# Kernel tuning notes

Hardware: AMD Instinct MI355X
Metric: run time of the kernel (lower is better)

The kernel has to match this reference:

```python
import jax, jax.numpy as jnp
import numpy as np

B = 131072           # batch of claims
PED = 256            # point_embedding_dim (divisible by 4)
NED = 128            # number_embedding_dim
CED = 512            # claim_embedding_dim
Q = PED // 4         # per sin/cos projection width
FEAT = 2 * PED + 3 * NED  # 896, MLP input


def setup_inputs() -> dict:
    key = jax.random.key(0)
    ks = list(jax.random.split(key, 48))
    it = iter(ks)

    def nrm(shape, s=0.1):
        return jax.random.normal(next(it), shape, jnp.float32) * s

    d = {
        "src_xy": jax.random.normal(next(it), (B, 2), jnp.float32),
        "dst_xy": jax.random.normal(next(it), (B, 2), jnp.float32),
        "time_s": jax.random.uniform(next(it), (B,), jnp.float32),
        "wait_src": jax.random.uniform(next(it), (B,), jnp.float32),
        "wait_dst": jax.random.uniform(next(it), (B,), jnp.float32),
    }
    # PointEncoder params: 4 Linear(1, Q) per encoder -> weight as vector [Q] + bias [Q]
    for pfx in ("src", "dst"):
        for part in ("wsx", "bsx", "wcx", "bcx", "wsy", "bsy", "wcy", "bcy"):
            d[f"{pfx}_{part}"] = nrm((Q,), 1.0 if part[0] == "w" else 0.1)
    # NumberEncoder params: Linear(1, NED)
    for pfx in ("t", "ws", "wd"):
        d[f"{pfx}_w"] = nrm((NED,), 1.0)
        d[f"{pfx}_b"] = nrm((NED,), 0.1)
    # MLP params
    d["W1"] = nrm((FEAT, CED), 0.03)
    d["b1"] = nrm((CED,), 0.01)
    d["W2"] = nrm((CED, CED), 0.04)
    d["b2"] = nrm((CED,), 0.01)
    return d


def _point_enc(xy, wsx, bsx, wcx, bcx, wsy, bsy, wcy, bcy):
    # xy: [B,2] -> [B, PED]
    x = xy[:, 0:1]
    y = xy[:, 1:2]
    return jnp.concatenate([
        jnp.sin(x * wsx + bsx),
        jnp.cos(x * wcx + bcx),
        jnp.sin(y * wsy + bsy),
        jnp.cos(y * wcy + bcy),
    ], axis=-1)


def _num_enc(t, w, b):
    # t: [B] -> [B, NED], LeakyReLU slope 0.01 (torch default)
    return jax.nn.leaky_relu(t[:, None] * w + b, 0.01)


def reference(src_xy, dst_xy, time_s, wait_src, wait_dst,
              src_wsx, src_bsx, src_wcx, src_bcx, src_wsy, src_bsy, src_wcy, src_bcy,
              dst_wsx, dst_bsx, dst_wcx, dst_bcx, dst_wsy, dst_bsy, dst_wcy, dst_bcy,
              t_w, t_b, ws_w, ws_b, wd_w, wd_b,
              W1, b1, W2, b2):
    feats = jnp.concatenate([
        _point_enc(src_xy, src_wsx, src_bsx, src_wcx, src_bcx,
                   src_wsy, src_bsy, src_wcy, src_bcy),
        _point_enc(dst_xy, dst_wsx, dst_bsx, dst_wcx, dst_bcx,
                   dst_wsy, dst_bsy, dst_wcy, dst_bcy),
        _num_enc(time_s, t_w, t_b),
        _num_enc(wait_src, ws_w, ws_b),
        _num_enc(wait_dst, wd_w, wd_b),
    ], axis=-1)  # [B, FEAT]
    h = jax.nn.leaky_relu(feats @ W1 + b1, 0.01)
    out = jax.nn.leaky_relu(h @ W2 + b2, 0.01)  # [B, CED]
    return out
```

## Files before the change

kernel.cpp:

```cpp
#include <hip/hip_runtime.h>
#include <stdint.h>

typedef __bf16 bf16x8 __attribute__((ext_vector_type(8)));
typedef float f32x4 __attribute__((ext_vector_type(4)));

#define AS1C(p) ((const __attribute__((address_space(1))) void*)(p))
#define AS3(p)  ((__attribute__((address_space(3))) void*)(p))

__device__ __forceinline__ unsigned short f2bf(float f) {
    unsigned int u = __float_as_uint(f);
    u += 0x7FFFu + ((u >> 16) & 1u);
    return (unsigned short)(u >> 16);
}
__device__ __forceinline__ float leaky(float v) { return v > 0.0f ? v : 0.01f * v; }

__global__ void k_transpose_bf16(const float* __restrict__ in, unsigned short* __restrict__ out,
                                 int K, int N) {
    int idx = blockIdx.x * 256 + threadIdx.x;
    if (idx >= K * N) return;
    int n = idx / K;
    int k = idx - n * K;
    out[idx] = f2bf(in[(size_t)k * N + n]);
}

__global__ void k_encode(
    const float* __restrict__ src_xy, const float* __restrict__ dst_xy,
    const float* __restrict__ time_s, const float* __restrict__ wait_src, const float* __restrict__ wait_dst,
    const float* __restrict__ s_wsx, const float* __restrict__ s_bsx,
    const float* __restrict__ s_wcx, const float* __restrict__ s_bcx,
    const float* __restrict__ s_wsy, const float* __restrict__ s_bsy,
    const float* __restrict__ s_wcy, const float* __restrict__ s_bcy,
    const float* __restrict__ d_wsx, const float* __restrict__ d_bsx,
    const float* __restrict__ d_wcx, const float* __restrict__ d_bcx,
    const float* __restrict__ d_wsy, const float* __restrict__ d_bsy,
    const float* __restrict__ d_wcy, const float* __restrict__ d_bcy,
    const float* __restrict__ t_w, const float* __restrict__ t_b,
    const float* __restrict__ ws_w, const float* __restrict__ ws_b,
    const float* __restrict__ wd_w, const float* __restrict__ wd_b,
    unsigned short* __restrict__ out, int rows) {
    unsigned int g = blockIdx.x * 256u + threadIdx.x;
    if (g >= (unsigned)rows * 112u) return;
    unsigned int row = g / 112u;
    int k0 = (int)(g - row * 112u) * 8;

    float v[8];
    if (k0 < 512) {
        const float* xy = (k0 < 256) ? src_xy : dst_xy;
        int local = k0 & 255;
        int seg = local >> 6;
        int j = local & 63;
        float sc = (seg < 2) ? xy[2 * row] : xy[2 * row + 1];
        const float* W;
        const float* Bv;
        if (k0 < 256) {
            W  = (seg == 0) ? s_wsx : (seg == 1) ? s_wcx : (seg == 2) ? s_wsy : s_wcy;
            Bv = (seg == 0) ? s_bsx : (seg == 1) ? s_bcx : (seg == 2) ? s_bsy : s_bcy;
        } else {
            W  = (seg == 0) ? d_wsx : (seg == 1) ? d_wcx : (seg == 2) ? d_wsy : d_wcy;
            Bv = (seg == 0) ? d_bsx : (seg == 1) ? d_bcx : (seg == 2) ? d_bsy : d_bcy;
        }
        bool isSin = ((seg & 1) == 0);
        float4 w0 = *(const float4*)&W[j],  w1 = *(const float4*)&W[j + 4];
        float4 b0 = *(const float4*)&Bv[j], b1v = *(const float4*)&Bv[j + 4];
        float wa[8] = {w0.x, w0.y, w0.z, w0.w, w1.x, w1.y, w1.z, w1.w};
        float ba[8] = {b0.x, b0.y, b0.z, b0.w, b1v.x, b1v.y, b1v.z, b1v.w};
#pragma unroll
        for (int i = 0; i < 8; ++i) {
            float a = fmaf(sc, wa[i], ba[i]);
            v[i] = isSin ? __sinf(a) : __cosf(a);
        }
    } else {
        int local = k0 - 512;
        int which = local >> 7;
        int j = local & 127;
        float s = (which == 0) ? time_s[row] : (which == 1) ? wait_src[row] : wait_dst[row];
        const float* W  = (which == 0) ? t_w : (which == 1) ? ws_w : wd_w;
        const float* Bv = (which == 0) ? t_b : (which == 1) ? ws_b : wd_b;
        float4 w0 = *(const float4*)&W[j],  w1 = *(const float4*)&W[j + 4];
        float4 b0 = *(const float4*)&Bv[j], b1v = *(const float4*)&Bv[j + 4];
        float wa[8] = {w0.x, w0.y, w0.z, w0.w, w1.x, w1.y, w1.z, w1.w};
        float ba[8] = {b0.x, b0.y, b0.z, b0.w, b1v.x, b1v.y, b1v.z, b1v.w};
#pragma unroll
        for (int i = 0; i < 8; ++i) {
            float a = fmaf(s, wa[i], ba[i]);
            v[i] = leaky(a);
        }
    }
    unsigned int p0 = (unsigned)f2bf(v[0]) | ((unsigned)f2bf(v[1]) << 16);
    unsigned int p1 = (unsigned)f2bf(v[2]) | ((unsigned)f2bf(v[3]) << 16);
    unsigned int p2 = (unsigned)f2bf(v[4]) | ((unsigned)f2bf(v[5]) << 16);
    unsigned int p3 = (unsigned)f2bf(v[6]) | ((unsigned)f2bf(v[7]) << 16);
    uint4 pk = {p0, p1, p2, p3};
    *reinterpret_cast<uint4*>(out + (size_t)row * 896u + (unsigned)k0) = pk;
}

template <int K, bool OUT_BF16>
__global__ void k_gemm(const unsigned short* __restrict__ A, const unsigned short* __restrict__ BT,
                       const float* __restrict__ bias, void* __restrict__ Cv) {
    __shared__ __align__(16) unsigned short lA[128 * 64];
    __shared__ __align__(16) unsigned short lB[128 * 64];

    const int tid = threadIdx.x;

    int nwg = gridDim.x, bid = blockIdx.x;
    int q = nwg >> 3, r = nwg & 7;
    int xcd = bid & 7, idx = bid >> 3;
    int swz = (xcd < r ? xcd * (q + 1) : r * (q + 1) + (xcd - r) * q) + idx;
    int mblk = swz >> 2, nblk = swz & 3;
    size_t brow = (size_t)mblk * 128;
    int bcol = nblk * 128;

    const int lane = tid & 63, w = tid >> 6;
    const int wr = w >> 1, wc = w & 1;
    const int lrow = lane & 15, kg = lane >> 4;

    f32x4 acc[4][4] = {};

    for (int kt = 0; kt < K / 64; ++kt) {
#pragma unroll
        for (int i = 0; i < 4; ++i) {
            int chunk = i * 256 + tid;
            int rr = chunk >> 3, cc = chunk & 7;
            __builtin_amdgcn_global_load_lds(AS1C(A + (brow + rr) * K + kt * 64 + cc * 8),
                                             AS3(lA + chunk * 8), 16, 0, 0);
            __builtin_amdgcn_global_load_lds(AS1C(BT + (size_t)(bcol + rr) * K + kt * 64 + cc * 8),
                                             AS3(lB + chunk * 8), 16, 0, 0);
        }
        __syncthreads();
#pragma unroll
        for (int kk = 0; kk < 2; ++kk) {
            bf16x8 af[4], bfr[4];
#pragma unroll
            for (int m = 0; m < 4; ++m)
                af[m] = *(const bf16x8*)&lA[(wr * 64 + m * 16 + lrow) * 64 + kk * 32 + kg * 8];
#pragma unroll
            for (int n = 0; n < 4; ++n)
                bfr[n] = *(const bf16x8*)&lB[(wc * 64 + n * 16 + lrow) * 64 + kk * 32 + kg * 8];
#pragma unroll
            for (int m = 0; m < 4; ++m)
#pragma unroll
                for (int n = 0; n < 4; ++n)
                    acc[m][n] = __builtin_amdgcn_mfma_f32_16x16x32_bf16(af[m], bfr[n], acc[m][n], 0, 0, 0);
        }
        __syncthreads();
    }

#pragma unroll
    for (int n = 0; n < 4; ++n) {
        int col = bcol + wc * 64 + n * 16 + lrow;
        float bn = bias[col];
#pragma unroll
        for (int m = 0; m < 4; ++m) {
            size_t row0 = brow + wr * 64 + m * 16 + kg * 4;
#pragma unroll
            for (int rg = 0; rg < 4; ++rg) {
                float vv = leaky(acc[m][n][rg] + bn);
                if (OUT_BF16)
                    ((unsigned short*)Cv)[(row0 + rg) * 512 + col] = f2bf(vv);
                else
                    ((float*)Cv)[(row0 + rg) * 512 + col] = vv;
            }
        }
    }
}

extern "C" void kernel_launch(void* const* d_in, const int* in_sizes, int n_in,
                              void* d_out, int out_size, void* d_ws, size_t ws_size,
                              hipStream_t stream) {
    const float* src_xy   = (const float*)d_in[0];
    const float* dst_xy   = (const float*)d_in[1];
    const float* time_s   = (const float*)d_in[2];
    const float* wait_src = (const float*)d_in[3];
    const float* wait_dst = (const float*)d_in[4];
    const float* sp[8]; for (int i = 0; i < 8; ++i) sp[i] = (const float*)d_in[5 + i];
    const float* dp[8]; for (int i = 0; i < 8; ++i) dp[i] = (const float*)d_in[13 + i];
    const float* t_w  = (const float*)d_in[21];
    const float* t_b  = (const float*)d_in[22];
    const float* ws_w = (const float*)d_in[23];
    const float* ws_b = (const float*)d_in[24];
    const float* wd_w = (const float*)d_in[25];
    const float* wd_b = (const float*)d_in[26];
    const float* W1 = (const float*)d_in[27];
    const float* b1 = (const float*)d_in[28];
    const float* W2 = (const float*)d_in[29];
    const float* b2 = (const float*)d_in[30];

    unsigned short* W1T = (unsigned short*)d_ws;
    unsigned short* W2T = (unsigned short*)((char*)d_ws + 917504);
    char* dyn = (char*)d_ws + 1441792;

    k_transpose_bf16<<<(896 * 512 + 255) / 256, 256, 0, stream>>>(W1, W1T, 896, 512);
    k_transpose_bf16<<<(512 * 512 + 255) / 256, 256, 0, stream>>>(W2, W2T, 512, 512);

    const int ROWS = 131072;
    size_t avail = ws_size > 1441792 ? ws_size - 1441792 : 0;
    int chunk = ROWS;
    while (chunk > 128 && (size_t)chunk * 2816 > avail) chunk >>= 1;

    for (int r0 = 0; r0 < ROWS; r0 += chunk) {
        unsigned short* feats = (unsigned short*)dyn;
        unsigned short* h = (unsigned short*)(dyn + (size_t)chunk * 1792);
        k_encode<<<(chunk * 112 + 255) / 256, 256, 0, stream>>>(
            src_xy + (size_t)r0 * 2, dst_xy + (size_t)r0 * 2,
            time_s + r0, wait_src + r0, wait_dst + r0,
            sp[0], sp[1], sp[2], sp[3], sp[4], sp[5], sp[6], sp[7],
            dp[0], dp[1], dp[2], dp[3], dp[4], dp[5], dp[6], dp[7],
            t_w, t_b, ws_w, ws_b, wd_w, wd_b, feats, chunk);
        k_gemm<896, true><<<(chunk / 128) * 4, 256, 0, stream>>>(feats, W1T, b1, (void*)h);
        k_gemm<512, false><<<(chunk / 128) * 4, 256, 0, stream>>>(h, W2T, b2,
                                                                  (void*)((float*)d_out + (size_t)r0 * 512));
    }
}
```

Before: 724.2 us.

## Fuse feature encoding and both MLP GEMMs into one kernel

Replaces the separate encode, GEMM1 and GEMM2 launches with a single kernel. Each 128-row block encodes its features on the fly into swizzled LDS, computes hidden tiles 128 columns at a time, and accumulates the second GEMM from LDS-resident hidden activations. This removes the HBM round trips for the bf16 feature and hidden matrices, which the old path wrote and reread. In exchange the encoding is recomputed once per hidden-column chunk, and the large LDS footprint limits occupancy.

```diff
diff --git a/kernel.cpp b/kernel.cpp
--- a/kernel.cpp
+++ b/kernel.cpp
@@ -13,6 +13,8 @@
     return (unsigned short)(u >> 16);
 }
 __device__ __forceinline__ float leaky(float v) { return v > 0.0f ? v : 0.01f * v; }
+__device__ __forceinline__ int swz7(int d) { return d ^ (((d >> 7) & 7) << 4); }
+__device__ __forceinline__ int swz8(int d) { return d ^ (((d >> 8) & 7) << 4); }
 
 __global__ void k_transpose_bf16(const float* __restrict__ in, unsigned short* __restrict__ out,
                                  int K, int N) {
@@ -23,143 +25,201 @@
     out[idx] = f2bf(in[(size_t)k * N + n]);
 }
 
-__global__ void k_encode(
-    const float* __restrict__ src_xy, const float* __restrict__ dst_xy,
-    const float* __restrict__ time_s, const float* __restrict__ wait_src, const float* __restrict__ wait_dst,
-    const float* __restrict__ s_wsx, const float* __restrict__ s_bsx,
-    const float* __restrict__ s_wcx, const float* __restrict__ s_bcx,
-    const float* __restrict__ s_wsy, const float* __restrict__ s_bsy,
-    const float* __restrict__ s_wcy, const float* __restrict__ s_bcy,
-    const float* __restrict__ d_wsx, const float* __restrict__ d_bsx,
-    const float* __restrict__ d_wcx, const float* __restrict__ d_bcx,
-    const float* __restrict__ d_wsy, const float* __restrict__ d_bsy,
-    const float* __restrict__ d_wcy, const float* __restrict__ d_bcy,
-    const float* __restrict__ t_w, const float* __restrict__ t_b,
-    const float* __restrict__ ws_w, const float* __restrict__ ws_b,
-    const float* __restrict__ wd_w, const float* __restrict__ wd_b,
-    unsigned short* __restrict__ out, int rows) {
-    unsigned int g = blockIdx.x * 256u + threadIdx.x;
-    if (g >= (unsigned)rows * 112u) return;
-    unsigned int row = g / 112u;
-    int k0 = (int)(g - row * 112u) * 8;
-
-    float v[8];
-    if (k0 < 512) {
-        const float* xy = (k0 < 256) ? src_xy : dst_xy;
-        int local = k0 & 255;
-        int seg = local >> 6;
-        int j = local & 63;
-        float sc = (seg < 2) ? xy[2 * row] : xy[2 * row + 1];
-        const float* W;
-        const float* Bv;
-        if (k0 < 256) {
-            W  = (seg == 0) ? s_wsx : (seg == 1) ? s_wcx : (seg == 2) ? s_wsy : s_wcy;
-            Bv = (seg == 0) ? s_bsx : (seg == 1) ? s_bcx : (seg == 2) ? s_bsy : s_bcy;
+struct KParams {
+    const float* src_xy; const float* dst_xy; const float* time_s;
+    const float* wait_src; const float* wait_dst;
+    const float* sp[8]; const float* dp[8];
+    const float* t_w; const float* t_b; const float* ws_w; const float* ws_b;
+    const float* wd_w; const float* wd_b;
+    const float* b1; const float* b2;
+    const unsigned short* W1T; const unsigned short* W2T;
+    float* out;
+};
+
+#define OF_SCAL 0
+#define OF_PAR  3584
+#define OF_F    10752
+#define OF_W    43520
+#define OF_H    109056
+#define LDS_TOT 141824
+
+__launch_bounds__(512, 2)
+__global__ void k_fused(KParams p) {
+    extern __shared__ char sm[];
+    float* scal = (float*)(sm + OF_SCAL);
+    float* par  = (float*)(sm + OF_PAR);
+
+    const int tid  = threadIdx.x;
+    const int lane = tid & 63, wid = tid >> 6;
+    const int lrow = lane & 15, kg = lane >> 4;
+    const int wr1 = wid >> 1, wc1 = wid & 1;
+    const int wr2 = wid >> 2, wc2 = wid & 3;
+
+    int swzb = (blockIdx.x & 7) * ((int)gridDim.x >> 3) + ((int)blockIdx.x >> 3);
+    const size_t brow = (size_t)swzb * 128;
+
+    for (int j = tid; j < 896; j += 512) {
+        int f = j >> 7, r = j & 127;
+        size_t gr = brow + r;
+        float v;
+        if      (f == 0) v = p.src_xy[2 * gr];
+        else if (f == 1) v = p.src_xy[2 * gr + 1];
+        else if (f == 2) v = p.dst_xy[2 * gr];
+        else if (f == 3) v = p.dst_xy[2 * gr + 1];
+        else if (f == 4) v = p.time_s[gr];
+        else if (f == 5) v = p.wait_src[gr];
+        else             v = p.wait_dst[gr];
+        scal[f * 128 + r] = v;
+    }
+    for (int j = tid; j < 1792; j += 512) {
+        int kt = j >> 7, rem = j & 127, isb = (rem >> 6) & 1, c = rem & 63;
+        float v;
+        if (kt < 8) {
+            const float* const* arr = (kt < 4) ? p.sp : p.dp;
+            v = arr[(kt & 3) * 2 + isb][c];
         } else {
-            W  = (seg == 0) ? d_wsx : (seg == 1) ? d_wcx : (seg == 2) ? d_wsy : d_wcy;
-            Bv = (seg == 0) ? d_bsx : (seg == 1) ? d_bcx : (seg == 2) ? d_bsy : d_bcy;
-        }
-        bool isSin = ((seg & 1) == 0);
-        float4 w0 = *(const float4*)&W[j],  w1 = *(const float4*)&W[j + 4];
-        float4 b0 = *(const float4*)&Bv[j], b1v = *(const float4*)&Bv[j + 4];
-        float wa[8] = {w0.x, w0.y, w0.z, w0.w, w1.x, w1.y, w1.z, w1.w};
-        float ba[8] = {b0.x, b0.y, b0.z, b0.w, b1v.x, b1v.y, b1v.z, b1v.w};
-#pragma unroll
-        for (int i = 0; i < 8; ++i) {
-            float a = fmaf(sc, wa[i], ba[i]);
-            v[i] = isSin ? __sinf(a) : __cosf(a);
-        }
-    } else {
-        int local = k0 - 512;
-        int which = local >> 7;
-        int j = local & 127;
-        float s = (which == 0) ? time_s[row] : (which == 1) ? wait_src[row] : wait_dst[row];
-        const float* W  = (which == 0) ? t_w : (which == 1) ? ws_w : wd_w;
-        const float* Bv = (which == 0) ? t_b : (which == 1) ? ws_b : wd_b;
-        float4 w0 = *(const float4*)&W[j],  w1 = *(const float4*)&W[j + 4];
-        float4 b0 = *(const float4*)&Bv[j], b1v = *(const float4*)&Bv[j + 4];
-        float wa[8] = {w0.x, w0.y, w0.z, w0.w, w1.x, w1.y, w1.z, w1.w};
-        float ba[8] = {b0.x, b0.y, b0.z, b0.w, b1v.x, b1v.y, b1v.z, b1v.w};
-#pragma unroll
-        for (int i = 0; i < 8; ++i) {
-            float a = fmaf(s, wa[i], ba[i]);
-            v[i] = leaky(a);
-        }
-    }
-    unsigned int p0 = (unsigned)f2bf(v[0]) | ((unsigned)f2bf(v[1]) << 16);
-    unsigned int p1 = (unsigned)f2bf(v[2]) | ((unsigned)f2bf(v[3]) << 16);
-    unsigned int p2 = (unsigned)f2bf(v[4]) | ((unsigned)f2bf(v[5]) << 16);
-    unsigned int p3 = (unsigned)f2bf(v[6]) | ((unsigned)f2bf(v[7]) << 16);
-    uint4 pk = {p0, p1, p2, p3};
-    *reinterpret_cast<uint4*>(out + (size_t)row * 896u + (unsigned)k0) = pk;
-}
-
-template <int K, bool OUT_BF16>
-__global__ void k_gemm(const unsigned short* __restrict__ A, const unsigned short* __restrict__ BT,
-                       const float* __restrict__ bias, void* __restrict__ Cv) {
-    __shared__ __align__(16) unsigned short lA[128 * 64];
-    __shared__ __align__(16) unsigned short lB[128 * 64];
-
-    const int tid = threadIdx.x;
-
-    int nwg = gridDim.x, bid = blockIdx.x;
-    int q = nwg >> 3, r = nwg & 7;
-    int xcd = bid & 7, idx = bid >> 3;
-    int swz = (xcd < r ? xcd * (q + 1) : r * (q + 1) + (xcd - r) * q) + idx;
-    int mblk = swz >> 2, nblk = swz & 3;
-    size_t brow = (size_t)mblk * 128;
-    int bcol = nblk * 128;
-
-    const int lane = tid & 63, w = tid >> 6;
-    const int wr = w >> 1, wc = w & 1;
-    const int lrow = lane & 15, kg = lane >> 4;
-
-    f32x4 acc[4][4] = {};
-
-    for (int kt = 0; kt < K / 64; ++kt) {
-#pragma unroll
-        for (int i = 0; i < 4; ++i) {
-            int chunk = i * 256 + tid;
-            int rr = chunk >> 3, cc = chunk & 7;
-            __builtin_amdgcn_global_load_lds(AS1C(A + (brow + rr) * K + kt * 64 + cc * 8),
-                                             AS3(lA + chunk * 8), 16, 0, 0);
-            __builtin_amdgcn_global_load_lds(AS1C(BT + (size_t)(bcol + rr) * K + kt * 64 + cc * 8),
-                                             AS3(lB + chunk * 8), 16, 0, 0);
-        }
+            int which = (kt - 8) >> 1;
+            const float* q = (which == 0) ? (isb ? p.t_b : p.t_w)
+                           : (which == 1) ? (isb ? p.ws_b : p.ws_w)
+                                          : (isb ? p.wd_b : p.wd_w);
+            v = q[((kt & 1) << 6) + c];
+        }
+        par[j] = v;
+    }
+
+    f32x4 oacc[4][8] = {};
+    __syncthreads();
+
+    auto encode = [&](int ke, char* dst) {
+        int r = tid >> 2, c0 = (tid & 3) << 4;
+        int sidx = (ke < 8) ? (((ke >> 2) << 1) + ((ke >> 1) & 1)) : (4 + ((ke - 8) >> 1));
+        float s = scal[sidx * 128 + r];
+        const float* wv = par + ke * 128;
+        const float* bv = wv + 64;
+        float val[16];
+        if (ke < 8) {
+            if (ke & 1) {
+#pragma unroll
+                for (int i = 0; i < 16; ++i) val[i] = __cosf(fmaf(s, wv[c0 + i], bv[c0 + i]));
+            } else {
+#pragma unroll
+                for (int i = 0; i < 16; ++i) val[i] = __sinf(fmaf(s, wv[c0 + i], bv[c0 + i]));
+            }
+        } else {
+#pragma unroll
+            for (int i = 0; i < 16; ++i) val[i] = leaky(fmaf(s, wv[c0 + i], bv[c0 + i]));
+        }
+        uint4 pk0, pk1;
+        pk0.x = (unsigned)f2bf(val[0])  | ((unsigned)f2bf(val[1])  << 16);
+        pk0.y = (unsigned)f2bf(val[2])  | ((unsigned)f2bf(val[3])  << 16);
+        pk0.z = (unsigned)f2bf(val[4])  | ((unsigned)f2bf(val[5])  << 16);
+        pk0.w = (unsigned)f2bf(val[6])  | ((unsigned)f2bf(val[7])  << 16);
+        pk1.x = (unsigned)f2bf(val[8])  | ((unsigned)f2bf(val[9])  << 16);
+        pk1.y = (unsigned)f2bf(val[10]) | ((unsigned)f2bf(val[11]) << 16);
+        pk1.z = (unsigned)f2bf(val[12]) | ((unsigned)f2bf(val[13]) << 16);
+        pk1.w = (unsigned)f2bf(val[14]) | ((unsigned)f2bf(val[15]) << 16);
+        int d = r * 128 + c0 * 2;
+        *(uint4*)(dst + swz7(d))      = pk0;
+        *(uint4*)(dst + swz7(d + 16)) = pk1;
+    };
+    auto stageW1 = [&](int nc, int kt) {
+        char* dst = sm + OF_W + (kt & 1) * 16384;
+#pragma unroll
+        for (int j = 0; j < 2; ++j) {
+            int d = tid * 16 + j * 8192;
+            int ds = swz7(d);
+            int r = ds >> 7, cb = ds & 127;
+            const unsigned short* src = p.W1T + (size_t)(nc * 128 + r) * 896 + kt * 64 + (cb >> 1);
+            __builtin_amdgcn_global_load_lds(AS1C(src), AS3(dst + d), 16, 0, 0);
+        }
+    };
+    auto stageW2 = [&](int nc, int k2) {
+        char* dst = sm + OF_W + (k2 & 1) * 32768;
+#pragma unroll
+        for (int j = 0; j < 4; ++j) {
+            int d = tid * 16 + j * 8192;
+            int ds = swz7(d);
+            int r = ds >> 6, cb = ds & 63;
+            const unsigned short* src = p.W2T + (size_t)r * 512 + nc * 128 + k2 * 32 + (cb >> 1);
+            __builtin_amdgcn_global_load_lds(AS1C(src), AS3(dst + d), 16, 0, 0);
+        }
+    };
+
+    for (int nc = 0; nc < 4; ++nc) {
+        stageW1(nc, 0);
+        encode(0, sm + OF_F);
+        f32x4 hacc[2][4] = {};
         __syncthreads();
-#pragma unroll
-        for (int kk = 0; kk < 2; ++kk) {
-            bf16x8 af[4], bfr[4];
+        for (int kt = 0; kt < 14; ++kt) {
+            char* fb = sm + OF_F + (kt & 1) * 16384;
+            char* wb = sm + OF_W + (kt & 1) * 16384;
+            if (kt < 13) {
+                stageW1(nc, kt + 1);
+                encode(kt + 1, sm + OF_F + ((kt + 1) & 1) * 16384);
+            }
+#pragma unroll
+            for (int kk = 0; kk < 2; ++kk) {
+                bf16x8 af[2], bfr[4];
+#pragma unroll
+                for (int m = 0; m < 2; ++m)
+                    af[m] = *(const bf16x8*)(fb + swz7((wr1 * 32 + m * 16 + lrow) * 128 + kk * 64 + kg * 16));
+#pragma unroll
+                for (int n = 0; n < 4; ++n)
+                    bfr[n] = *(const bf16x8*)(wb + swz7((wc1 * 64 + n * 16 + lrow) * 128 + kk * 64 + kg * 16));
+#pragma unroll
+                for (int m = 0; m < 2; ++m)
+#pragma unroll
+                    for (int n = 0; n < 4; ++n)
+                        hacc[m][n] = __builtin_amdgcn_mfma_f32_16x16x32_bf16(af[m], bfr[n], hacc[m][n], 0, 0, 0);
+            }
+            __syncthreads();
+        }
+        stageW2(nc, 0);
+        {
+            float b1v[4];
+#pragma unroll
+            for (int n = 0; n < 4; ++n) b1v[n] = p.b1[nc * 128 + wc1 * 64 + n * 16 + lrow];
+#pragma unroll
+            for (int m = 0; m < 2; ++m)
+#pragma unroll
+                for (int n = 0; n < 4; ++n)
+#pragma unroll
+                    for (int rg = 0; rg < 4; ++rg) {
+                        int hr = wr1 * 32 + m * 16 + kg * 4 + rg;
+                        int hc = wc1 * 64 + n * 16 + lrow;
+                        *(unsigned short*)(sm + OF_H + swz8(hr * 256 + hc * 2)) =
+                            f2bf(leaky(hacc[m][n][rg] + b1v[n]));
+                    }
+        }
+        __syncthreads();
+        for (int k2 = 0; k2 < 4; ++k2) {
+            char* wb = sm + OF_W + (k2 & 1) * 32768;
+            if (k2 < 3) stageW2(nc, k2 + 1);
+            bf16x8 ha[4], wfr[8];
 #pragma unroll
             for (int m = 0; m < 4; ++m)
-                af[m] = *(const bf16x8*)&lA[(wr * 64 + m * 16 + lrow) * 64 + kk * 32 + kg * 8];
-#pragma unroll
-            for (int n = 0; n < 4; ++n)
-                bfr[n] = *(const bf16x8*)&lB[(wc * 64 + n * 16 + lrow) * 64 + kk * 32 + kg * 8];
+                ha[m] = *(const bf16x8*)(sm + OF_H + swz8((wr2 * 64 + m * 16 + lrow) * 256 + k2 * 64 + kg * 16));
+#pragma unroll
+            for (int n = 0; n < 8; ++n)
+                wfr[n] = *(const bf16x8*)(wb + swz7((wc2 * 128 + n * 16 + lrow) * 64 + kg * 16));
 #pragma unroll
             for (int m = 0; m < 4; ++m)
 #pragma unroll
-                for (int n = 0; n < 4; ++n)
-                    acc[m][n] = __builtin_amdgcn_mfma_f32_16x16x32_bf16(af[m], bfr[n], acc[m][n], 0, 0, 0);
-        }
-        __syncthreads();
-    }
-
-#pragma unroll
-    for (int n = 0; n < 4; ++n) {
-        int col = bcol + wc * 64 + n * 16 + lrow;
-        float bn = bias[col];
+                for (int n = 0; n < 8; ++n)
+                    oacc[m][n] = __builtin_amdgcn_mfma_f32_16x16x32_bf16(ha[m], wfr[n], oacc[m][n], 0, 0, 0);
+            __syncthreads();
+        }
+    }
+#pragma unroll
+    for (int n = 0; n < 8; ++n) {
+        int col = wc2 * 128 + n * 16 + lrow;
+        float b2v = p.b2[col];
 #pragma unroll
         for (int m = 0; m < 4; ++m) {
-            size_t row0 = brow + wr * 64 + m * 16 + kg * 4;
-#pragma unroll
-            for (int rg = 0; rg < 4; ++rg) {
-                float vv = leaky(acc[m][n][rg] + bn);
-                if (OUT_BF16)
-                    ((unsigned short*)Cv)[(row0 + rg) * 512 + col] = f2bf(vv);
-                else
-                    ((float*)Cv)[(row0 + rg) * 512 + col] = vv;
-            }
+            size_t row0 = brow + wr2 * 64 + m * 16 + kg * 4;
+#pragma unroll
+            for (int rg = 0; rg < 4; ++rg)
+                p.out[(row0 + rg) * 512 + col] = leaky(oacc[m][n][rg] + b2v);
         }
     }
 }
@@ -167,47 +227,35 @@
 extern "C" void kernel_launch(void* const* d_in, const int* in_sizes, int n_in,
                               void* d_out, int out_size, void* d_ws, size_t ws_size,
                               hipStream_t stream) {
-    const float* src_xy   = (const float*)d_in[0];
-    const float* dst_xy   = (const float*)d_in[1];
-    const float* time_s   = (const float*)d_in[2];
-    const float* wait_src = (const float*)d_in[3];
-    const float* wait_dst = (const float*)d_in[4];
-    const float* sp[8]; for (int i = 0; i < 8; ++i) sp[i] = (const float*)d_in[5 + i];
-    const float* dp[8]; for (int i = 0; i < 8; ++i) dp[i] = (const float*)d_in[13 + i];
-    const float* t_w  = (const float*)d_in[21];
-    const float* t_b  = (const float*)d_in[22];
-    const float* ws_w = (const float*)d_in[23];
-    const float* ws_b = (const float*)d_in[24];
-    const float* wd_w = (const float*)d_in[25];
-    const float* wd_b = (const float*)d_in[26];
+    KParams kp;
+    kp.src_xy   = (const float*)d_in[0];
+    kp.dst_xy   = (const float*)d_in[1];
+    kp.time_s   = (const float*)d_in[2];
+    kp.wait_src = (const float*)d_in[3];
+    kp.wait_dst = (const float*)d_in[4];
+    for (int i = 0; i < 8; ++i) kp.sp[i] = (const float*)d_in[5 + i];
+    for (int i = 0; i < 8; ++i) kp.dp[i] = (const float*)d_in[13 + i];
+    kp.t_w  = (const float*)d_in[21];
+    kp.t_b  = (const float*)d_in[22];
+    kp.ws_w = (const float*)d_in[23];
+    kp.ws_b = (const float*)d_in[24];
+    kp.wd_w = (const float*)d_in[25];
+    kp.wd_b = (const float*)d_in[26];
     const float* W1 = (const float*)d_in[27];
-    const float* b1 = (const float*)d_in[28];
+    kp.b1 = (const float*)d_in[28];
     const float* W2 = (const float*)d_in[29];
-    const float* b2 = (const float*)d_in[30];
+    kp.b2 = (const float*)d_in[30];
+    kp.out = (float*)d_out;
 
     unsigned short* W1T = (unsigned short*)d_ws;
     unsigned short* W2T = (unsigned short*)((char*)d_ws + 917504);
-    char* dyn = (char*)d_ws + 1441792;
+    kp.W1T = W1T;
+    kp.W2T = W2T;
 
     k_transpose_bf16<<<(896 * 512 + 255) / 256, 256, 0, stream>>>(W1, W1T, 896, 512);
     k_transpose_bf16<<<(512 * 512 + 255) / 256, 256, 0, stream>>>(W2, W2T, 512, 512);
 
-    const int ROWS = 131072;
-    size_t avail = ws_size > 1441792 ? ws_size - 1441792 : 0;
-    int chunk = ROWS;
-    while (chunk > 128 && (size_t)chunk * 2816 > avail) chunk >>= 1;
-
-    for (int r0 = 0; r0 < ROWS; r0 += chunk) {
-        unsigned short* feats = (unsigned short*)dyn;
-        unsigned short* h = (unsigned short*)(dyn + (size_t)chunk * 1792);
-        k_encode<<<(chunk * 112 + 255) / 256, 256, 0, stream>>>(
-            src_xy + (size_t)r0 * 2, dst_xy + (size_t)r0 * 2,
-            time_s + r0, wait_src + r0, wait_dst + r0,
-            sp[0], sp[1], sp[2], sp[3], sp[4], sp[5], sp[6], sp[7],
-            dp[0], dp[1], dp[2], dp[3], dp[4], dp[5], dp[6], dp[7],
-            t_w, t_b, ws_w, ws_b, wd_w, wd_b, feats, chunk);
-        k_gemm<896, true><<<(chunk / 128) * 4, 256, 0, stream>>>(feats, W1T, b1, (void*)h);
-        k_gemm<512, false><<<(chunk / 128) * 4, 256, 0, stream>>>(h, W2T, b2,
-                                                                  (void*)((float*)d_out + (size_t)r0 * 512));
-    }
-}
+    hipFuncSetAttribute((const void*)k_fused,
+                        hipFuncAttributeMaxDynamicSharedMemorySize, LDS_TOT);
+    k_fused<<<1024, 512, LDS_TOT, stream>>>(kp);
+}
```

Result: slower. 770.9 us (+6.5%).
